# Optimization experiments

Hardware: AMD Instinct MI355X
Metric: run time of the kernel (lower is better)

The kernel has to match this reference:

```python
import jax, jax.numpy as jnp
import numpy as np

B, T, D, H = 4, 1024, 1024, 16
DH = D // H
NEG_BIG = jnp.float32(-2.0**32 + 1)


def layer_norm(x, scale, bias, eps=1e-5):
    mean = jnp.mean(x, axis=-1, keepdims=True)
    var = jnp.mean(jnp.square(x - mean), axis=-1, keepdims=True)
    return (x - mean) * jax.lax.rsqrt(var + eps) * scale + bias


def setup_inputs() -> dict:
    key = jax.random.key(0)
    ks = jax.random.split(key, 10)
    s = 0.02
    x = jax.random.normal(ks[0], (B, T, D), jnp.float32)
    mask = jax.random.randint(ks[1], (B, T), 0, 2).astype(jnp.float32)
    return {
        "x": x,
        "mask": mask,
        "wq": jax.random.normal(ks[2], (D, D), jnp.float32) * s,
        "wk": jax.random.normal(ks[3], (D, D), jnp.float32) * s,
        "wv": jax.random.normal(ks[4], (D, D), jnp.float32) * s,
        "w1": jax.random.normal(ks[5], (D, D), jnp.float32) * s,
        "b1": jnp.zeros((D,), jnp.float32),
        "w2": jax.random.normal(ks[6], (D, D), jnp.float32) * s,
        "b2": jnp.zeros((D,), jnp.float32),
        "ln1_s": jnp.ones((D,), jnp.float32),
        "ln1_b": jnp.zeros((D,), jnp.float32),
        "ln2_s": jnp.ones((D,), jnp.float32),
        "ln2_b": jnp.zeros((D,), jnp.float32),
        "ln3_s": jnp.ones((D,), jnp.float32),
        "ln3_b": jnp.zeros((D,), jnp.float32),
    }


def _mask_enc(x, mask, wq, wk, wv, w1, b1, w2, b2,
              ln1_s, ln1_b, ln2_s, ln2_b, ln3_s, ln3_b):
    b, t, d = x.shape
    # --- multi-head attention (hand-rolled, matches torch split/cat trick) ---
    Q = (x @ wq).reshape(b, t, H, DH).transpose(0, 2, 1, 3)  # [B,H,T,dh]
    K = (x @ wk).reshape(b, t, H, DH).transpose(0, 2, 1, 3)
    V = (x @ wv).reshape(b, t, H, DH).transpose(0, 2, 1, 3)
    scores = jnp.einsum('bhqd,bhkd->bhqk', Q, K) / jnp.sqrt(jnp.float32(DH))
    # key padding mask from sign of |K| row sums
    key_m = jnp.sign(jnp.sum(jnp.abs(K), axis=-1))  # [B,H,T]
    scores = jnp.where(key_m[:, :, None, :] == 0, NEG_BIG, scores)
    # FORWARD direction: allowed where col_index > row_index (strict)
    idx = jnp.arange(t)
    allowed = (idx[None, :] > idx[:, None]).astype(scores.dtype)  # [T,T]
    scores = scores + (1.0 - allowed) * (-10000.0)
    attn = jax.nn.softmax(scores, axis=-1)
    # post-softmax query mask multiply
    query_m = jnp.sign(jnp.sum(jnp.abs(Q), axis=-1))[:, :, :, None]  # [B,H,T,1]
    attn = attn * query_m
    out = jnp.einsum('bhqk,bhkd->bhqd', attn, V)
    out = out.transpose(0, 2, 1, 3).reshape(b, t, d)  # combine heads
    out = out * mask[:, :, None]
    # --- residual + layernorm wrapper (attention) ---
    h1 = layer_norm(x + out, ln1_s, ln1_b)
    # --- FFN + residual + layernorm ---
    ffn = jax.nn.relu(h1 @ w1 + b1) @ w2 + b2
    h2 = layer_norm(h1 + ffn, ln2_s, ln2_b)
    # --- output normalization ---
    return layer_norm(h2, ln3_s, ln3_b)


def reference(x, mask, wq, wk, wv, w1, b1, w2, b2,
              ln1_s, ln1_b, ln2_s, ln2_b, ln3_s, ln3_b):
    return _mask_enc(x, mask, wq, wk, wv, w1, b1, w2, b2,
                     ln1_s, ln1_b, ln2_s, ln2_b, ln3_s, ln3_b)
```

## Files before the change

kernel.cpp:

```cpp
#include <hip/hip_runtime.h>
#include <stdint.h>


#define B_  4
#define T_  1024
#define D_  1024
#define H_  16
#define DH_ 64

typedef __attribute__((ext_vector_type(8))) short short8;
typedef __attribute__((ext_vector_type(4))) float floatx4;
typedef __attribute__((ext_vector_type(4))) _Float16 half4;

__device__ __forceinline__ unsigned short f2bf(float f) {
  union { float f; uint32_t u; } a; a.f = f;
  uint32_t r = a.u + 0x7FFFu + ((a.u >> 16) & 1u);
  return (unsigned short)(r >> 16);
}
__device__ __forceinline__ float bf2f(unsigned short u) {
  union { uint32_t u; float f; } a; a.u = ((uint32_t)u) << 16;
  return a.f;
}

#define GLD_LDS16(g, l) __builtin_amdgcn_global_load_lds( \
    (const __attribute__((address_space(1))) unsigned int*)(g), \
    (__attribute__((address_space(3))) unsigned int*)(l), 16, 0, 0)

__global__ __launch_bounds__(256)
void prep_kernel(const float4* __restrict__ x4, unsigned short* __restrict__ xb,
                 const float* __restrict__ w0, const float* __restrict__ w1,
                 const float* __restrict__ w2, const float* __restrict__ w3,
                 const float* __restrict__ w4, unsigned short* __restrict__ dst_all) {
  const int t = threadIdx.x;
  if (blockIdx.x < 1024) {
    int idx0 = blockIdx.x * 1024 + t;
#pragma unroll
    for (int c = 0; c < 4; ++c) {
      int idx = idx0 + c * 256;
      float4 v = x4[idx];
      union { uint2 u; unsigned short s[4]; } o;
      o.s[0] = f2bf(v.x); o.s[1] = f2bf(v.y); o.s[2] = f2bf(v.z); o.s[3] = f2bf(v.w);
      *(uint2*)&xb[(size_t)idx * 4] = o.u;
    }
    return;
  }
  const int b = blockIdx.x - 1024;
  const int z = b >> 8, ky = (b >> 4) & 15, nx = b & 15;
  const float* src = (z == 0) ? w0 : (z == 1) ? w1 : (z == 2) ? w2 : (z == 3) ? w3 : w4;
  unsigned short* dst = dst_all + (size_t)z * D_ * D_;
  __shared__ __align__(16) unsigned short tile[64 * 72];
  const int k0 = ky * 64, n0 = nx * 64;
#pragma unroll
  for (int c = 0; c < 4; ++c) {
    int idx = c * 256 + t;
    int r = idx >> 4, cc = (idx & 15) << 2;
    float4 v = *(const float4*)&src[(size_t)(k0 + r) * D_ + n0 + cc];
    tile[(cc + 0) * 72 + r] = f2bf(v.x);
    tile[(cc + 1) * 72 + r] = f2bf(v.y);
    tile[(cc + 2) * 72 + r] = f2bf(v.z);
    tile[(cc + 3) * 72 + r] = f2bf(v.w);
  }
  __syncthreads();
  int rr = t >> 2, ck = (t & 3) << 4;
  uint4 v0 = *(const uint4*)&tile[rr * 72 + ck];
  uint4 v1 = *(const uint4*)&tile[rr * 72 + ck + 8];
  *(uint4*)&dst[(size_t)(n0 + rr) * D_ + k0 + ck] = v0;
  *(uint4*)&dst[(size_t)(n0 + rr) * D_ + k0 + ck + 8] = v1;
}

__global__ __launch_bounds__(256, 2)
void gemm_qkv(const unsigned short* __restrict__ A,
              const unsigned short* __restrict__ Bt,
              unsigned short* __restrict__ oQ, unsigned short* __restrict__ oK,
              _Float16* __restrict__ oV) {
  const int K = 1024;
  __shared__ __align__(16) unsigned char smem[34816];
  unsigned short* As = (unsigned short*)smem;
  unsigned short* Bs = (unsigned short*)(smem + 16384);
  _Float16* Cs = (_Float16*)smem;
  const int t = threadIdx.x;
  const int lane = t & 63, w = t >> 6;
  const int quad = lane >> 4, lm = lane & 15;
  const int wm = w >> 1, wn = w & 1;
  const int m0 = blockIdx.y * 128, n0 = blockIdx.x * 128;
  const int srow = lane >> 3;
  const int scol = ((lane & 7) ^ srow) << 3;

  floatx4 acc[4][4];
#pragma unroll
  for (int i = 0; i < 4; ++i)
#pragma unroll
    for (int j = 0; j < 4; ++j) acc[i][j] = (floatx4){0.f, 0.f, 0.f, 0.f};

  for (int kt = 0; kt < K; kt += 64) {
#pragma unroll
    for (int i = 0; i < 4; ++i) {
      const unsigned short* ga = A + (size_t)(m0 + w * 32 + i * 8 + srow) * K + kt + scol;
      const unsigned short* gb = Bt + (size_t)(n0 + w * 32 + i * 8 + srow) * K + kt + scol;
      GLD_LDS16(ga, &As[w * 2048 + i * 512]);
      GLD_LDS16(gb, &Bs[w * 2048 + i * 512]);
    }
    __syncthreads();
#pragma unroll
    for (int ks = 0; ks < 2; ++ks) {
      const int rs = ((ks * 4 + quad) ^ (lm & 7)) << 3;
      short8 a[4], b[4];
#pragma unroll
      for (int i = 0; i < 4; ++i) a[i] = *(const short8*)&As[(wm * 64 + i * 16 + lm) * 64 + rs];
#pragma unroll
      for (int j = 0; j < 4; ++j) b[j] = *(const short8*)&Bs[(wn * 64 + j * 16 + lm) * 64 + rs];
#pragma unroll
      for (int i = 0; i < 4; ++i)
#pragma unroll
        for (int j = 0; j < 4; ++j)
          acc[i][j] = __builtin_amdgcn_mfma_f32_16x16x32_bf16(a[i], b[j], acc[i][j], 0, 0, 0);
    }
    __syncthreads();
  }

  if (n0 < 2048) {
    unsigned short* p = (n0 < 1024) ? oQ : oK;
    const float qscale = (n0 < 1024) ? 0.18033688f : 1.0f;
#pragma unroll
    for (int i = 0; i < 4; ++i) {
      int gmb = m0 + wm * 64 + i * 16 + quad * 4;
#pragma unroll
      for (int j = 0; j < 4; ++j) {
        int gn = n0 + wn * 64 + j * 16 + lm;
        int nn = gn & 1023, hh = nn >> 6, dd = nn & 63;
#pragma unroll
        for (int r = 0; r < 4; ++r) {
          int gm = gmb + r;
          int bb = gm >> 10, tt = gm & 1023;
          p[(((size_t)bb * H_ + hh) * T_ + tt) * DH_ + dd] = f2bf(acc[i][j][r] * qscale);
        }
      }
    }
  } else {
#pragma unroll
    for (int i = 0; i < 4; ++i) {
#pragma unroll
      for (int j = 0; j < 4; ++j) {
        int gn = n0 + wn * 64 + j * 16 + lm;
        int hd = (gn >> 6) & 1, dd = gn & 63;
        int kperm = quad * 32 + (wm * 4 + i) * 4;
        union { _Float16 h[4]; uint2 u; } pk;
#pragma unroll
        for (int r = 0; r < 4; ++r) pk.h[r] = (_Float16)acc[i][j][r];
        *(uint2*)&Cs[((size_t)(hd * 64 + dd)) * 136 + kperm] = pk.u;
      }
    }
    __syncthreads();
    const int row = t >> 1, half = t & 1;
    const int hd = row >> 6, dd = row & 63;
    const int hh = ((n0 & 1023) >> 6) + hd;
    const int bb = m0 >> 10, kbg = (m0 >> 7) & 7;
    const _Float16* srcp = &Cs[(size_t)(hd * 64 + dd) * 136 + half * 64];
    _Float16* dstp = oV + ((((size_t)bb * H_ + hh) * DH_ + dd) * 8 + kbg) * 128 + half * 64;
#pragma unroll
    for (int g = 0; g < 8; ++g)
      *(uint4*)(dstp + g * 8) = *(const uint4*)(srcp + g * 8);
  }
}

template <int MODE>
__global__ __launch_bounds__(256, 2)
void gemm_ffn(const unsigned short* __restrict__ A,
              const unsigned short* __restrict__ Bt,
              unsigned short* __restrict__ oBf,
              const float* __restrict__ bias) {
  const int K = 1024, N = 1024;
  __shared__ __align__(16) unsigned short As[64 * 64];
  __shared__ __align__(16) unsigned short Bs[128 * 64];
  const int t = threadIdx.x;
  const int lane = t & 63, w = t >> 6;
  const int quad = lane >> 4, lm = lane & 15;
  const int wm = w >> 1, wn = w & 1;
  const int m0 = blockIdx.y * 64, n0 = blockIdx.x * 128;
  const int srow = lane >> 3;
  const int scol = ((lane & 7) ^ srow) << 3;

  floatx4 acc[2][4];
#pragma unroll
  for (int i = 0; i < 2; ++i)
#pragma unroll
    for (int j = 0; j < 4; ++j) acc[i][j] = (floatx4){0.f, 0.f, 0.f, 0.f};

  for (int kt = 0; kt < K; kt += 64) {
#pragma unroll
    for (int i = 0; i < 2; ++i) {
      const unsigned short* ga = A + (size_t)(m0 + w * 16 + i * 8 + srow) * K + kt + scol;
      GLD_LDS16(ga, &As[w * 1024 + i * 512]);
    }
#pragma unroll
    for (int i = 0; i < 4; ++i) {
      const unsigned short* gb = Bt + (size_t)(n0 + w * 32 + i * 8 + srow) * K + kt + scol;
      GLD_LDS16(gb, &Bs[w * 2048 + i * 512]);
    }
    __syncthreads();
#pragma unroll
    for (int ks = 0; ks < 2; ++ks) {
      const int rs = ((ks * 4 + quad) ^ (lm & 7)) << 3;
      short8 a[2], b[4];
#pragma unroll
      for (int i = 0; i < 2; ++i) a[i] = *(const short8*)&As[(wm * 32 + i * 16 + lm) * 64 + rs];
#pragma unroll
      for (int j = 0; j < 4; ++j) b[j] = *(const short8*)&Bs[(wn * 64 + j * 16 + lm) * 64 + rs];
#pragma unroll
      for (int i = 0; i < 2; ++i)
#pragma unroll
        for (int j = 0; j < 4; ++j)
          acc[i][j] = __builtin_amdgcn_mfma_f32_16x16x32_bf16(a[i], b[j], acc[i][j], 0, 0, 0);
    }
    __syncthreads();
  }

#pragma unroll
  for (int i = 0; i < 2; ++i) {
    int gmb = m0 + wm * 32 + i * 16 + quad * 4;
#pragma unroll
    for (int j = 0; j < 4; ++j) {
      int gn = n0 + wn * 64 + j * 16 + lm;
      float bv = bias[gn];
#pragma unroll
      for (int r = 0; r < 4; ++r) {
        int gm = gmb + r;
        float v = acc[i][j][r] + bv;
        if (MODE == 1) v = fmaxf(v, 0.f);
        oBf[(size_t)gm * N + gn] = f2bf(v);
      }
    }
  }
}

__global__ __launch_bounds__(256)
void flash_attn(const unsigned short* __restrict__ Qb,
                const unsigned short* __restrict__ Kb,
                const _Float16* __restrict__ Vtg,
                const float* __restrict__ maskp,
                unsigned short* __restrict__ attn) {
  __shared__ __align__(16) unsigned short KLs[2][8192];
  __shared__ __align__(16) _Float16      VLs[2][8192];

  const int t = threadIdx.x;
  const int lane = t & 63, w = t >> 6;
  const int quad = lane >> 4, lm = lane & 15;

  const int bid = blockIdx.x;
  const int hi  = bid >> 8;
  const int lo  = bid & 255;
  const int xcd = lo & 7;
  const int hgrp = (lo >> 3) & 7;
  const int qpair = lo >> 6;
  const int qb = hi ? (7 - qpair) : qpair;
  const int head = hgrp * 8 + xcd;
  const int hh = head & 15, bb = head >> 4;
  const int q0 = qb << 7;

  const size_t headoff = ((size_t)bb * H_ + hh) * T_ * DH_;
  const unsigned short* Qh = Qb + headoff;
  const unsigned short* Kh = Kb + headoff;
  const _Float16* Vh = Vtg + headoff;

  short8 qf[2][2];
#pragma unroll
  for (int qg = 0; qg < 2; ++qg)
#pragma unroll
    for (int ks = 0; ks < 2; ++ks)
      qf[qg][ks] = *(const short8*)(Qh + (size_t)(q0 + w * 32 + qg * 16 + lm) * 64 + ks * 32 + quad * 8);

  float lsum[2] = {0.f, 0.f};
  floatx4 acc[2][4];
#pragma unroll
  for (int qg = 0; qg < 2; ++qg)
#pragma unroll
    for (int j2 = 0; j2 < 4; ++j2) acc[qg][j2] = (floatx4){0.f, 0.f, 0.f, 0.f};

  const int qglob0 = q0 + w * 32 + lm;
  const bool excl1 = (qglob0 + 16 == 1023);
  const float MSHIFT = 14426.950408f;

  const int my_lo  = (qb == 7 && w == 3) ? 0 : qb;
  const int blk_lo = (qb == 7) ? 0 : qb;

  const unsigned short* gk[4];
  const _Float16* gv[4];
#pragma unroll
  for (int i = 0; i < 4; ++i) {
    int s = w * 4 + i;
    gk[i] = Kh + (size_t)((s >> 1) * 16 + lm) * 64 + (s & 1) * 32 + quad * 8;
    gv[i] = Vh + ((size_t)((s >> 2) * 16 + lm) * 8) * 128 + quad * 32 + (s & 3) * 8;
  }

#pragma unroll
  for (int i = 0; i < 4; ++i) {
    int s = w * 4 + i;
    GLD_LDS16(gk[i] + (size_t)blk_lo * 8192, &KLs[0][s * 512]);
    GLD_LDS16(gv[i] + (size_t)blk_lo * 128,  &VLs[0][s * 512]);
  }

  int cur = 0;
  for (int kb = blk_lo; kb < 8; ++kb) {
    __syncthreads();
    if (kb + 1 < 8) {
      int nxt = cur ^ 1;
#pragma unroll
      for (int i = 0; i < 4; ++i) {
        int s = w * 4 + i;
        GLD_LDS16(gk[i] + (size_t)(kb + 1) * 8192, &KLs[nxt][s * 512]);
        GLD_LDS16(gv[i] + (size_t)(kb + 1) * 128,  &VLs[nxt][s * 512]);
      }
    }
    if (kb >= my_lo) {
      const unsigned short* Kc = &KLs[cur][0];
      const _Float16* Vc = &VLs[cur][0];
      const int k0 = kb * 128;
      const bool need_mask = (kb <= qb);

      short8 kA = *(const short8*)&Kc[(0 * 64 + lane) * 8];
      short8 kB = *(const short8*)&Kc[(1 * 64 + lane) * 8];
      half4 vA0 = *(const half4*)&Vc[((0 * 4 + 0) * 64 + lane) * 8];
      half4 vA1 = *(const half4*)&Vc[((1 * 4 + 0) * 64 + lane) * 8];
      half4 vA2 = *(const half4*)&Vc[((2 * 4 + 0) * 64 + lane) * 8];
      half4 vA3 = *(const half4*)&Vc[((3 * 4 + 0) * 64 + lane) * 8];

#pragma unroll
      for (int j = 0; j < 8; ++j) {
        short8 nA, nB; half4 n0, n1, n2, n3;
        if (j < 7) {
          int jn = j + 1;
          nA = *(const short8*)&Kc[((jn * 2 + 0) * 64 + lane) * 8];
          nB = *(const short8*)&Kc[((jn * 2 + 1) * 64 + lane) * 8];
          n0 = *(const half4*)&Vc[((0 * 4 + (jn >> 1)) * 64 + lane) * 8 + (jn & 1) * 4];
          n1 = *(const half4*)&Vc[((1 * 4 + (jn >> 1)) * 64 + lane) * 8 + (jn & 1) * 4];
          n2 = *(const half4*)&Vc[((2 * 4 + (jn >> 1)) * 64 + lane) * 8 + (jn & 1) * 4];
          n3 = *(const half4*)&Vc[((3 * 4 + (jn >> 1)) * 64 + lane) * 8 + (jn & 1) * 4];
        }
        floatx4 st[2];
#pragma unroll
        for (int qg = 0; qg < 2; ++qg) {
          floatx4 z = (floatx4){0.f, 0.f, 0.f, 0.f};
          z = __builtin_amdgcn_mfma_f32_16x16x32_bf16(kA, qf[qg][0], z, 0, 0, 0);
          st[qg] = __builtin_amdgcn_mfma_f32_16x16x32_bf16(kB, qf[qg][1], z, 0, 0, 0);
        }
        half4 pa[2];
#pragma unroll
        for (int qg = 0; qg < 2; ++qg) {
          const int qq = qglob0 + qg * 16;
          const bool skip = (qg == 1) && excl1;
#pragma unroll
          for (int r = 0; r < 4; ++r) {
            int kg = k0 + j * 16 + quad * 4 + r;
            float v = st[qg][r];
            if (need_mask && !skip && kg <= qq) v -= MSHIFT;
            float p = __builtin_amdgcn_exp2f(v);
            lsum[qg] += p;
            pa[qg][r] = (_Float16)p;
          }
        }
        acc[0][0] = __builtin_amdgcn_mfma_f32_16x16x16f16(pa[0], vA0, acc[0][0], 0, 0, 0);
        acc[1][0] = __builtin_amdgcn_mfma_f32_16x16x16f16(pa[1], vA0, acc[1][0], 0, 0, 0);
        acc[0][1] = __builtin_amdgcn_mfma_f32_16x16x16f16(pa[0], vA1, acc[0][1], 0, 0, 0);
        acc[1][1] = __builtin_amdgcn_mfma_f32_16x16x16f16(pa[1], vA1, acc[1][1], 0, 0, 0);
        acc[0][2] = __builtin_amdgcn_mfma_f32_16x16x16f16(pa[0], vA2, acc[0][2], 0, 0, 0);
        acc[1][2] = __builtin_amdgcn_mfma_f32_16x16x16f16(pa[1], vA2, acc[1][2], 0, 0, 0);
        acc[0][3] = __builtin_amdgcn_mfma_f32_16x16x16f16(pa[0], vA3, acc[0][3], 0, 0, 0);
        acc[1][3] = __builtin_amdgcn_mfma_f32_16x16x16f16(pa[1], vA3, acc[1][3], 0, 0, 0);
        kA = nA; kB = nB; vA0 = n0; vA1 = n1; vA2 = n2; vA3 = n3;
      }
    }
    cur ^= 1;
  }

#pragma unroll
  for (int qg = 0; qg < 2; ++qg) {
    float l = lsum[qg];
    l += __shfl_xor(l, 16);
    l += __shfl_xor(l, 32);
    float s = maskp[bb * T_ + qglob0 + qg * 16] / l;
#pragma unroll
    for (int r = 0; r < 4; ++r) {
      float bsc = __shfl(s, quad * 4 + r);
      int tq = q0 + w * 32 + qg * 16 + quad * 4 + r;
#pragma unroll
      for (int j2 = 0; j2 < 4; ++j2)
        attn[((size_t)(bb * T_ + tq)) * D_ + hh * 64 + j2 * 16 + lm] = f2bf(acc[qg][j2][r] * bsc);
    }
  }
}

__global__ __launch_bounds__(256)
void ln_res_kernel(const unsigned short* __restrict__ xb, const unsigned short* __restrict__ attn,
                   const float* __restrict__ sc, const float* __restrict__ bi,
                   unsigned short* __restrict__ hb) {
  const int t = threadIdx.x;
  const int lane = t & 63, w = t >> 6;
  const int row = blockIdx.x * 4 + w;
  const size_t base = (size_t)row * D_ + lane * 16;

  float v[16];
  float s1 = 0.f, s2 = 0.f;
#pragma unroll
  for (int i = 0; i < 4; ++i) {
    union { uint2 u; unsigned short s[4]; } xu, au;
    xu.u = *(const uint2*)&xb[base + i * 4];
    au.u = *(const uint2*)&attn[base + i * 4];
    float x0 = bf2f(xu.s[0]) + bf2f(au.s[0]);
    float x1 = bf2f(xu.s[1]) + bf2f(au.s[1]);
    float x2 = bf2f(xu.s[2]) + bf2f(au.s[2]);
    float x3 = bf2f(xu.s[3]) + bf2f(au.s[3]);
    v[i * 4 + 0] = x0; v[i * 4 + 1] = x1; v[i * 4 + 2] = x2; v[i * 4 + 3] = x3;
    s1 += x0 + x1 + x2 + x3;
    s2 += x0 * x0 + x1 * x1 + x2 * x2 + x3 * x3;
  }
#pragma unroll
  for (int off = 1; off < 64; off <<= 1) {
    s1 += __shfl_xor(s1, off);
    s2 += __shfl_xor(s2, off);
  }
  float mean = s1 * (1.f / 1024.f);
  float var = s2 * (1.f / 1024.f) - mean * mean;
  float rstd = rsqrtf(var + 1e-5f);
#pragma unroll
  for (int i = 0; i < 4; ++i) {
    float4 sv = *(const float4*)&sc[lane * 16 + i * 4];
    float4 bv = *(const float4*)&bi[lane * 16 + i * 4];
    float o0 = (v[i * 4 + 0] - mean) * rstd * sv.x + bv.x;
    float o1 = (v[i * 4 + 1] - mean) * rstd * sv.y + bv.y;
    float o2 = (v[i * 4 + 2] - mean) * rstd * sv.z + bv.z;
    float o3 = (v[i * 4 + 3] - mean) * rstd * sv.w + bv.w;
    union { uint2 u; unsigned short s[4]; } ob;
    ob.s[0] = f2bf(o0); ob.s[1] = f2bf(o1); ob.s[2] = f2bf(o2); ob.s[3] = f2bf(o3);
    *(uint2*)&hb[base + i * 4] = ob.u;
  }
}

__global__ __launch_bounds__(256)
void ln_double_kernel(const unsigned short* __restrict__ h1b,
                      const unsigned short* __restrict__ ffnb,
                      const float* __restrict__ s2c, const float* __restrict__ b2c,
                      const float* __restrict__ s3c, const float* __restrict__ b3c,
                      float* __restrict__ out) {
  const int t = threadIdx.x;
  const int lane = t & 63, w = t >> 6;
  const int row = blockIdx.x * 4 + w;
  const size_t base = (size_t)row * D_ + lane * 16;

  float v[16];
  float s1 = 0.f, s2 = 0.f;
#pragma unroll
  for (int i = 0; i < 4; ++i) {
    union { uint2 u; unsigned short s[4]; } hu, fu;
    hu.u = *(const uint2*)&h1b[base + i * 4];
    fu.u = *(const uint2*)&ffnb[base + i * 4];
    float x0 = bf2f(hu.s[0]) + bf2f(fu.s[0]);
    float x1 = bf2f(hu.s[1]) + bf2f(fu.s[1]);
    float x2 = bf2f(hu.s[2]) + bf2f(fu.s[2]);
    float x3 = bf2f(hu.s[3]) + bf2f(fu.s[3]);
    v[i * 4 + 0] = x0; v[i * 4 + 1] = x1; v[i * 4 + 2] = x2; v[i * 4 + 3] = x3;
    s1 += x0 + x1 + x2 + x3;
    s2 += x0 * x0 + x1 * x1 + x2 * x2 + x3 * x3;
  }
#pragma unroll
  for (int off = 1; off < 64; off <<= 1) {
    s1 += __shfl_xor(s1, off);
    s2 += __shfl_xor(s2, off);
  }
  float mean = s1 * (1.f / 1024.f);
  float var = s2 * (1.f / 1024.f) - mean * mean;
  float rstd = rsqrtf(var + 1e-5f);

  float o[16];
  float u1 = 0.f, u2 = 0.f;
#pragma unroll
  for (int i = 0; i < 4; ++i) {
    float4 sv = *(const float4*)&s2c[lane * 16 + i * 4];
    float4 bv = *(const float4*)&b2c[lane * 16 + i * 4];
    float o0 = (v[i * 4 + 0] - mean) * rstd * sv.x + bv.x;
    float o1 = (v[i * 4 + 1] - mean) * rstd * sv.y + bv.y;
    float o2 = (v[i * 4 + 2] - mean) * rstd * sv.z + bv.z;
    float o3 = (v[i * 4 + 3] - mean) * rstd * sv.w + bv.w;
    o[i * 4 + 0] = o0; o[i * 4 + 1] = o1; o[i * 4 + 2] = o2; o[i * 4 + 3] = o3;
    u1 += o0 + o1 + o2 + o3;
    u2 += o0 * o0 + o1 * o1 + o2 * o2 + o3 * o3;
  }
#pragma unroll
  for (int off = 1; off < 64; off <<= 1) {
    u1 += __shfl_xor(u1, off);
    u2 += __shfl_xor(u2, off);
  }
  float mean2 = u1 * (1.f / 1024.f);
  float var2 = u2 * (1.f / 1024.f) - mean2 * mean2;
  float rstd2 = rsqrtf(var2 + 1e-5f);
#pragma unroll
  for (int i = 0; i < 4; ++i) {
    float4 sv = *(const float4*)&s3c[lane * 16 + i * 4];
    float4 bv = *(const float4*)&b3c[lane * 16 + i * 4];
    float4 fo;
    fo.x = (o[i * 4 + 0] - mean2) * rstd2 * sv.x + bv.x;
    fo.y = (o[i * 4 + 1] - mean2) * rstd2 * sv.y + bv.y;
    fo.z = (o[i * 4 + 2] - mean2) * rstd2 * sv.z + bv.z;
    fo.w = (o[i * 4 + 3] - mean2) * rstd2 * sv.w + bv.w;
    *(float4*)&out[base + i * 4] = fo;
  }
}

extern "C" void kernel_launch(void* const* d_in, const int* in_sizes, int n_in,
                              void* d_out, int out_size, void* d_ws, size_t ws_size,
                              hipStream_t stream) {
  (void)in_sizes; (void)n_in; (void)out_size; (void)ws_size;
  const float* x   = (const float*)d_in[0];
  const float* msk = (const float*)d_in[1];
  const float* wq  = (const float*)d_in[2];
  const float* wk  = (const float*)d_in[3];
  const float* wv  = (const float*)d_in[4];
  const float* w1  = (const float*)d_in[5];
  const float* b1  = (const float*)d_in[6];
  const float* w2  = (const float*)d_in[7];
  const float* b2  = (const float*)d_in[8];
  const float* l1s = (const float*)d_in[9];
  const float* l1b = (const float*)d_in[10];
  const float* l2s = (const float*)d_in[11];
  const float* l2b = (const float*)d_in[12];
  const float* l3s = (const float*)d_in[13];
  const float* l3b = (const float*)d_in[14];
  float* outp = (float*)d_out;

  char* ws = (char*)d_ws;
  unsigned short* xb   = (unsigned short*)(ws);
  unsigned short* wt   = (unsigned short*)(ws + ((size_t)8  << 20));
  unsigned short* Qb   = (unsigned short*)(ws + ((size_t)18 << 20));
  unsigned short* Kb   = (unsigned short*)(ws + ((size_t)26 << 20));
  _Float16*       Vtg  = (_Float16*)(ws + ((size_t)34 << 20));
  unsigned short* attn = (unsigned short*)(ws + ((size_t)42 << 20));
  unsigned short* h1b  = (unsigned short*)(ws + ((size_t)18 << 20));
  unsigned short* gb   = (unsigned short*)(ws + ((size_t)26 << 20));
  unsigned short* ffnb = (unsigned short*)(ws + ((size_t)34 << 20));

  prep_kernel<<<1024 + 1280, 256, 0, stream>>>((const float4*)x, xb,
                                               wq, wk, wv, w1, w2, wt);
  gemm_qkv<<<dim3(24, 32), 256, 0, stream>>>(xb, wt, Qb, Kb, Vtg);
  flash_attn<<<512, 256, 0, stream>>>(Qb, Kb, Vtg, msk, attn);
  ln_res_kernel<<<1024, 256, 0, stream>>>(xb, attn, l1s, l1b, h1b);
  gemm_ffn<1><<<dim3(8, 64), 256, 0, stream>>>(h1b, wt + (size_t)3 * 1024 * 1024, gb, b1);
  gemm_ffn<2><<<dim3(8, 64), 256, 0, stream>>>(gb, wt + (size_t)4 * 1024 * 1024, ffnb, b2);
  ln_double_kernel<<<1024, 256, 0, stream>>>(h1b, ffnb, l2s, l2b, l3s, l3b, outp);
}
```

Measured before the change: 222.1 us.

## Split flash attention query tile across eight waves of sixteen rows each

The attention kernel now launches 512 threads per block. Each of 8 waves handles 16 query rows instead of 4 waves handling 32, and the per-wave K/V LDS staging load drops from 4 slices to 2. This halves per-wave accumulator and register use to raise occupancy and latency hiding. In exchange, each K/V fragment read from LDS now feeds only one query group instead of two, so LDS read traffic per MFMA doubles.

```diff
diff --git a/kernel.cpp b/kernel.cpp
--- a/kernel.cpp
+++ b/kernel.cpp
@@ -233,7 +233,7 @@
   }
 }
 
-__global__ __launch_bounds__(256)
+__global__ __launch_bounds__(512)
 void flash_attn(const unsigned short* __restrict__ Qb,
                 const unsigned short* __restrict__ Kb,
                 const _Float16* __restrict__ Vtg,
@@ -262,39 +262,35 @@
   const unsigned short* Kh = Kb + headoff;
   const _Float16* Vh = Vtg + headoff;
 
-  short8 qf[2][2];
-#pragma unroll
-  for (int qg = 0; qg < 2; ++qg)
-#pragma unroll
-    for (int ks = 0; ks < 2; ++ks)
-      qf[qg][ks] = *(const short8*)(Qh + (size_t)(q0 + w * 32 + qg * 16 + lm) * 64 + ks * 32 + quad * 8);
-
-  float lsum[2] = {0.f, 0.f};
-  floatx4 acc[2][4];
-#pragma unroll
-  for (int qg = 0; qg < 2; ++qg)
-#pragma unroll
-    for (int j2 = 0; j2 < 4; ++j2) acc[qg][j2] = (floatx4){0.f, 0.f, 0.f, 0.f};
-
-  const int qglob0 = q0 + w * 32 + lm;
-  const bool excl1 = (qglob0 + 16 == 1023);
+  short8 qf[2];
+#pragma unroll
+  for (int ks = 0; ks < 2; ++ks)
+    qf[ks] = *(const short8*)(Qh + (size_t)(q0 + w * 16 + lm) * 64 + ks * 32 + quad * 8);
+
+  float lsum = 0.f;
+  floatx4 acc[4];
+#pragma unroll
+  for (int j2 = 0; j2 < 4; ++j2) acc[j2] = (floatx4){0.f, 0.f, 0.f, 0.f};
+
+  const int qglob = q0 + w * 16 + lm;
+  const bool excl = (qglob == 1023);
   const float MSHIFT = 14426.950408f;
 
-  const int my_lo  = (qb == 7 && w == 3) ? 0 : qb;
+  const int my_lo  = (qb == 7 && w == 7) ? 0 : qb;
   const int blk_lo = (qb == 7) ? 0 : qb;
 
-  const unsigned short* gk[4];
-  const _Float16* gv[4];
-#pragma unroll
-  for (int i = 0; i < 4; ++i) {
-    int s = w * 4 + i;
+  const unsigned short* gk[2];
+  const _Float16* gv[2];
+#pragma unroll
+  for (int i = 0; i < 2; ++i) {
+    int s = w * 2 + i;
     gk[i] = Kh + (size_t)((s >> 1) * 16 + lm) * 64 + (s & 1) * 32 + quad * 8;
     gv[i] = Vh + ((size_t)((s >> 2) * 16 + lm) * 8) * 128 + quad * 32 + (s & 3) * 8;
   }
 
 #pragma unroll
-  for (int i = 0; i < 4; ++i) {
-    int s = w * 4 + i;
+  for (int i = 0; i < 2; ++i) {
+    int s = w * 2 + i;
     GLD_LDS16(gk[i] + (size_t)blk_lo * 8192, &KLs[0][s * 512]);
     GLD_LDS16(gv[i] + (size_t)blk_lo * 128,  &VLs[0][s * 512]);
   }
@@ -305,8 +301,8 @@
     if (kb + 1 < 8) {
       int nxt = cur ^ 1;
 #pragma unroll
-      for (int i = 0; i < 4; ++i) {
-        int s = w * 4 + i;
+      for (int i = 0; i < 2; ++i) {
+        int s = w * 2 + i;
         GLD_LDS16(gk[i] + (size_t)(kb + 1) * 8192, &KLs[nxt][s * 512]);
         GLD_LDS16(gv[i] + (size_t)(kb + 1) * 128,  &VLs[nxt][s * 512]);
       }
@@ -336,55 +332,44 @@
           n2 = *(const half4*)&Vc[((2 * 4 + (jn >> 1)) * 64 + lane) * 8 + (jn & 1) * 4];
           n3 = *(const half4*)&Vc[((3 * 4 + (jn >> 1)) * 64 + lane) * 8 + (jn & 1) * 4];
         }
-        floatx4 st[2];
-#pragma unroll
-        for (int qg = 0; qg < 2; ++qg) {
+        floatx4 st;
+        {
           floatx4 z = (floatx4){0.f, 0.f, 0.f, 0.f};
-          z = __builtin_amdgcn_mfma_f32_16x16x32_bf16(kA, qf[qg][0], z, 0, 0, 0);
-          st[qg] = __builtin_amdgcn_mfma_f32_16x16x32_bf16(kB, qf[qg][1], z, 0, 0, 0);
+          z = __builtin_amdgcn_mfma_f32_16x16x32_bf16(kA, qf[0], z, 0, 0, 0);
+          st = __builtin_amdgcn_mfma_f32_16x16x32_bf16(kB, qf[1], z, 0, 0, 0);
         }
-        half4 pa[2];
-#pragma unroll
-        for (int qg = 0; qg < 2; ++qg) {
-          const int qq = qglob0 + qg * 16;
-          const bool skip = (qg == 1) && excl1;
-#pragma unroll
-          for (int r = 0; r < 4; ++r) {
-            int kg = k0 + j * 16 + quad * 4 + r;
-            float v = st[qg][r];
-            if (need_mask && !skip && kg <= qq) v -= MSHIFT;
-            float p = __builtin_amdgcn_exp2f(v);
-            lsum[qg] += p;
-            pa[qg][r] = (_Float16)p;
-          }
+        half4 pa;
+#pragma unroll
+        for (int r = 0; r < 4; ++r) {
+          int kg = k0 + j * 16 + quad * 4 + r;
+          float v = st[r];
+          if (need_mask && !excl && kg <= qglob) v -= MSHIFT;
+          float p = __builtin_amdgcn_exp2f(v);
+          lsum += p;
+          pa[r] = (_Float16)p;
         }
-        acc[0][0] = __builtin_amdgcn_mfma_f32_16x16x16f16(pa[0], vA0, acc[0][0], 0, 0, 0);
-        acc[1][0] = __builtin_amdgcn_mfma_f32_16x16x16f16(pa[1], vA0, acc[1][0], 0, 0, 0);
-        acc[0][1] = __builtin_amdgcn_mfma_f32_16x16x16f16(pa[0], vA1, acc[0][1], 0, 0, 0);
-        acc[1][1] = __builtin_amdgcn_mfma_f32_16x16x16f16(pa[1], vA1, acc[1][1], 0, 0, 0);
-        acc[0][2] = __builtin_amdgcn_mfma_f32_16x16x16f16(pa[0], vA2, acc[0][2], 0, 0, 0);
-        acc[1][2] = __builtin_amdgcn_mfma_f32_16x16x16f16(pa[1], vA2, acc[1][2], 0, 0, 0);
-        acc[0][3] = __builtin_amdgcn_mfma_f32_16x16x16f16(pa[0], vA3, acc[0][3], 0, 0, 0);
-        acc[1][3] = __builtin_amdgcn_mfma_f32_16x16x16f16(pa[1], vA3, acc[1][3], 0, 0, 0);
+        acc[0] = __builtin_amdgcn_mfma_f32_16x16x16f16(pa, vA0, acc[0], 0, 0, 0);
+        acc[1] = __builtin_amdgcn_mfma_f32_16x16x16f16(pa, vA1, acc[1], 0, 0, 0);
+        acc[2] = __builtin_amdgcn_mfma_f32_16x16x16f16(pa, vA2, acc[2], 0, 0, 0);
+        acc[3] = __builtin_amdgcn_mfma_f32_16x16x16f16(pa, vA3, acc[3], 0, 0, 0);
         kA = nA; kB = nB; vA0 = n0; vA1 = n1; vA2 = n2; vA3 = n3;
       }
     }
     cur ^= 1;
   }
 
-#pragma unroll
-  for (int qg = 0; qg < 2; ++qg) {
-    float l = lsum[qg];
+  {
+    float l = lsum;
     l += __shfl_xor(l, 16);
     l += __shfl_xor(l, 32);
-    float s = maskp[bb * T_ + qglob0 + qg * 16] / l;
+    float s = maskp[bb * T_ + qglob] / l;
 #pragma unroll
     for (int r = 0; r < 4; ++r) {
       float bsc = __shfl(s, quad * 4 + r);
-      int tq = q0 + w * 32 + qg * 16 + quad * 4 + r;
+      int tq = q0 + w * 16 + quad * 4 + r;
 #pragma unroll
       for (int j2 = 0; j2 < 4; ++j2)
-        attn[((size_t)(bb * T_ + tq)) * D_ + hh * 64 + j2 * 16 + lm] = f2bf(acc[qg][j2][r] * bsc);
+        attn[((size_t)(bb * T_ + tq)) * D_ + hh * 64 + j2 * 16 + lm] = f2bf(acc[j2][r] * bsc);
     }
   }
 }
@@ -540,7 +525,7 @@
   prep_kernel<<<1024 + 1280, 256, 0, stream>>>((const float4*)x, xb,
                                                wq, wk, wv, w1, w2, wt);
   gemm_qkv<<<dim3(24, 32), 256, 0, stream>>>(xb, wt, Qb, Kb, Vtg);
-  flash_attn<<<512, 256, 0, stream>>>(Qb, Kb, Vtg, msk, attn);
+  flash_attn<<<512, 512, 0, stream>>>(Qb, Kb, Vtg, msk, attn);
   ln_res_kernel<<<1024, 256, 0, stream>>>(xb, attn, l1s, l1b, h1b);
   gemm_ffn<1><<<dim3(8, 64), 256, 0, stream>>>(h1b, wt + (size_t)3 * 1024 * 1024, gb, b1);
   gemm_ffn<2><<<dim3(8, 64), 256, 0, stream>>>(gb, wt + (size_t)4 * 1024 * 1024, ffnb, b2);
```

Result: faster. 215.2 us (-3.1%).
